# Kernel optimization log

Hardware: AMD Instinct MI355X
Metric: run time of the kernel (lower is better)

Reference implementation:

```python
import jax, jax.numpy as jnp
import numpy as np

N_NODES = 50000
N_EDGES = 600000
D_IN = 128
D_HID = 128


def _sage_conv(x, src, dst, n_nodes, W_l, b_l, W_r):
    """PyG SAGEConv: out = lin_l(mean_j x_j) + lin_r(x_i); lin_r has no bias."""
    msg = x[src]  # [E, D] gather from source nodes
    agg = jax.ops.segment_sum(msg, dst, num_segments=n_nodes)
    cnt = jax.ops.segment_sum(jnp.ones((msg.shape[0],), x.dtype), dst,
                              num_segments=n_nodes)
    mean = agg / jnp.maximum(cnt, 1.0)[:, None]
    return mean @ W_l + b_l + x @ W_r


def setup_inputs() -> dict:
    key = jax.random.key(0)
    ks = jax.random.split(key, 8)
    x = jax.random.normal(ks[0], (N_NODES, D_IN), dtype=jnp.float32)
    edge_index = jax.random.randint(ks[1], (2, N_EDGES), 0, N_NODES, dtype=jnp.int64)
    s1 = 1.0 / np.sqrt(D_IN)
    s2 = 1.0 / np.sqrt(D_HID)
    W1_l = jax.random.uniform(ks[2], (D_IN, D_HID), jnp.float32, -s1, s1)
    W1_r = jax.random.uniform(ks[3], (D_IN, D_HID), jnp.float32, -s1, s1)
    b1_l = jnp.zeros((D_HID,), jnp.float32)
    W2_l = jax.random.uniform(ks[4], (D_HID, D_HID), jnp.float32, -s2, s2)
    W2_r = jax.random.uniform(ks[5], (D_HID, D_HID), jnp.float32, -s2, s2)
    b2_l = jnp.zeros((D_HID,), jnp.float32)
    return {"x": x, "edge_index": edge_index,
            "W1_l": W1_l, "b1_l": b1_l, "W1_r": W1_r,
            "W2_l": W2_l, "b2_l": b2_l, "W2_r": W2_r}


def reference(x, edge_index, W1_l, b1_l, W1_r, W2_l, b2_l, W2_r):
    # forward (eval mode: dropout is identity)
    src, dst = edge_index[0], edge_index[1]
    n = x.shape[0]
    z = jax.nn.relu(_sage_conv(x, src, dst, n, W1_l, b1_l, W1_r))
    z = _sage_conv(z, src, dst, n, W2_l, b2_l, W2_r)
    return z
```

## Files before the change

### kernel.cpp

```cpp
#include <hip/hip_runtime.h>

typedef unsigned short ushort_t;
typedef __attribute__((ext_vector_type(8))) unsigned short ushort8;
typedef __attribute__((ext_vector_type(8))) __bf16 bf16x8;
typedef __attribute__((ext_vector_type(4))) float f32x4;

#define CAP 128

__device__ __forceinline__ ushort_t f2bf(float f) {
    union { float f; unsigned u; } v; v.f = f;
    unsigned r = v.u + 0x7FFFu + ((v.u >> 16) & 1u);
    return (ushort_t)(r >> 16);
}
__device__ __forceinline__ float bf2f(ushort_t b) {
    union { unsigned u; float f; } v; v.u = ((unsigned)b) << 16;
    return v.f;
}

__global__ __launch_bounds__(256) void prep_kernel(
    const float* __restrict__ x, ushort_t* __restrict__ xb,
    const float* __restrict__ W1l, const float* __restrict__ W1r,
    const float* __restrict__ W2l, const float* __restrict__ W2r,
    ushort_t* __restrict__ WT1, ushort_t* __restrict__ WT2,
    int* __restrict__ cnt, int n8, int n)
{
    int gid = blockIdx.x * 256 + threadIdx.x;
    if (gid < n) cnt[gid] = 0;
    if (gid < 65536) {
        int layer = gid >> 15;
        int id = gid & 32767;
        int k = id >> 7;
        int c = id & 127;
        const float* Wl = layer ? W2l : W1l;
        const float* Wr = layer ? W2r : W1r;
        ushort_t* WT = layer ? WT2 : WT1;
        float v = (k < 128) ? Wl[(size_t)k * 128 + c] : Wr[(size_t)(k - 128) * 128 + c];
        WT[(size_t)c * 256 + k] = f2bf(v);
    }
    if (gid >= n8) return;
    const float4 v0 = *(const float4*)&x[(size_t)gid * 8];
    const float4 v1 = *(const float4*)&x[(size_t)gid * 8 + 4];
    ushort8 r;
    r[0] = f2bf(v0.x); r[1] = f2bf(v0.y); r[2] = f2bf(v0.z); r[3] = f2bf(v0.w);
    r[4] = f2bf(v1.x); r[5] = f2bf(v1.y); r[6] = f2bf(v1.z); r[7] = f2bf(v1.w);
    *(ushort8*)&xb[(size_t)gid * 8] = r;
}

__global__ __launch_bounds__(256) void fill_bucket(
    const int* __restrict__ src, const int* __restrict__ dst,
    int* __restrict__ cnt, int* __restrict__ esrc, int E)
{
    int e = blockIdx.x * 256 + threadIdx.x;
    if (e < E) {
        int d = dst[e];
        int pos = atomicAdd(&cnt[d], 1);
        if (pos < CAP) esrc[(size_t)d * CAP + pos] = src[e];
    }
}

__global__ __launch_bounds__(256) void sage_layer(
    const ushort_t* __restrict__ feat,
    const int* __restrict__ esrc,
    const int* __restrict__ cnt,
    const ushort_t* __restrict__ WT,
    const float* __restrict__ bias,
    ushort_t* __restrict__ out_b,
    float* __restrict__ out_f,
    int n, int do_relu)
{
    __shared__ __align__(16) ushort_t a_lds[64 * 256];

    const int t = threadIdx.x;
    const int tile = blockIdx.x * 64;
    const int w = t >> 6;
    const int l = t & 63;
    const int l15 = l & 15;
    const int lg = l >> 4;

#pragma unroll
    for (int j = 0; j < 4; ++j) {
        int idx = t + j * 256;
        int r = idx >> 4;
        int g = 16 + (idx & 15);
        int gr = tile + r;
        ushort8 v = (ushort8)0;
        if (gr < n) v = *(const ushort8*)&feat[(size_t)gr * 128 + (idx & 15) * 8];
        int dstb = r * 512 + ((g * 16) ^ ((r & 7) << 4));
        *(ushort8*)((char*)a_lds + dstb) = v;
    }

    const int slot = lg;
    const int c = l15 << 3;
    for (int i = 0; i < 16; ++i) {
        int r = w * 16 + i;
        int node = tile + r;
        float a[8];
#pragma unroll
        for (int j = 0; j < 8; ++j) a[j] = 0.f;
        int d = 0;
        if (node < n) d = min(cnt[node], CAP);
        const size_t o = (size_t)node * CAP;

        for (int base = 0; base < d; base += 64) {
            const int m = min(d - base, 64);
            int idxv = (l < m) ? esrc[o + base + l] : 0;
            const int nit = (m + 3) >> 2;
            for (int ii = 0; ii < nit; ii += 4) {
                int e0 = (ii + 0) * 4 + slot;
                int e1 = (ii + 1) * 4 + slot;
                int e2 = (ii + 2) * 4 + slot;
                int e3 = (ii + 3) * 4 + slot;
                int s0 = __shfl(idxv, e0 & 63, 64);
                int s1 = __shfl(idxv, e1 & 63, 64);
                int s2 = __shfl(idxv, e2 & 63, 64);
                int s3 = __shfl(idxv, e3 & 63, 64);
                ushort8 r0 = *(const ushort8*)&feat[(size_t)s0 * 128 + c];
                ushort8 r1 = *(const ushort8*)&feat[(size_t)s1 * 128 + c];
                ushort8 r2 = *(const ushort8*)&feat[(size_t)s2 * 128 + c];
                ushort8 r3 = *(const ushort8*)&feat[(size_t)s3 * 128 + c];
                if (e0 < m) {
#pragma unroll
                    for (int j = 0; j < 8; ++j) a[j] += bf2f(r0[j]);
                }
                if (e1 < m) {
#pragma unroll
                    for (int j = 0; j < 8; ++j) a[j] += bf2f(r1[j]);
                }
                if (e2 < m) {
#pragma unroll
                    for (int j = 0; j < 8; ++j) a[j] += bf2f(r2[j]);
                }
                if (e3 < m) {
#pragma unroll
                    for (int j = 0; j < 8; ++j) a[j] += bf2f(r3[j]);
                }
            }
        }

#pragma unroll
        for (int j = 0; j < 8; ++j) {
            a[j] += __shfl_xor(a[j], 16, 64);
            a[j] += __shfl_xor(a[j], 32, 64);
        }

        if (slot == 0) {
            float sc = 1.0f / fmaxf((float)d, 1.0f);
            ushort8 rv;
#pragma unroll
            for (int j = 0; j < 8; ++j) rv[j] = f2bf(a[j] * sc);
            int dstb = r * 512 + ((l15 * 16) ^ ((r & 7) << 4));
            *(ushort8*)((char*)a_lds + dstb) = rv;
        }
    }
    __syncthreads();

    bf16x8 bfrag[2][8];
    {
        const ushort_t* p0 = &WT[(size_t)(w * 32 + l15) * 256 + lg * 8];
        const ushort_t* p1 = p0 + 16 * 256;
#pragma unroll
        for (int ks = 0; ks < 8; ++ks) {
            bfrag[0][ks] = *(const bf16x8*)(p0 + ks * 32);
            bfrag[1][ks] = *(const bf16x8*)(p1 + ks * 32);
        }
    }

    f32x4 acc[4][2];
#pragma unroll
    for (int rt = 0; rt < 4; ++rt)
#pragma unroll
        for (int ct = 0; ct < 2; ++ct)
#pragma unroll
            for (int i = 0; i < 4; ++i) acc[rt][ct][i] = 0.f;

#pragma unroll
    for (int ks = 0; ks < 8; ++ks) {
        bf16x8 af[4];
#pragma unroll
        for (int rt = 0; rt < 4; ++rt) {
            int r = rt * 16 + l15;
            int byteoff = r * 512 + (((ks * 64) + lg * 16) ^ ((r & 7) << 4));
            af[rt] = *(const bf16x8*)((const char*)a_lds + byteoff);
        }
#pragma unroll
        for (int rt = 0; rt < 4; ++rt)
#pragma unroll
            for (int ct = 0; ct < 2; ++ct)
                acc[rt][ct] = __builtin_amdgcn_mfma_f32_16x16x32_bf16(
                    af[rt], bfrag[ct][ks], acc[rt][ct], 0, 0, 0);
    }

#pragma unroll
    for (int ct = 0; ct < 2; ++ct) {
        int col = w * 32 + ct * 16 + l15;
        float bv = bias[col];
#pragma unroll
        for (int rt = 0; rt < 4; ++rt) {
#pragma unroll
            for (int i = 0; i < 4; ++i) {
                int row = tile + rt * 16 + lg * 4 + i;
                if (row < n) {
                    float v = acc[rt][ct][i] + bv;
                    if (do_relu) v = fmaxf(v, 0.f);
                    if (out_b) out_b[(size_t)row * 128 + col] = f2bf(v);
                    else       out_f[(size_t)row * 128 + col] = v;
                }
            }
        }
    }
}

extern "C" void kernel_launch(void* const* d_in, const int* in_sizes, int n_in,
                              void* d_out, int out_size, void* d_ws, size_t ws_size,
                              hipStream_t stream) {
    const float* x   = (const float*)d_in[0];
    const int*   ei  = (const int*)d_in[1];
    const float* W1l = (const float*)d_in[2];
    const float* b1l = (const float*)d_in[3];
    const float* W1r = (const float*)d_in[4];
    const float* W2l = (const float*)d_in[5];
    const float* b2l = (const float*)d_in[6];
    const float* W2r = (const float*)d_in[7];
    float* out = (float*)d_out;

    const int N = in_sizes[0] / 128;
    const int E = in_sizes[1] / 2;
    const int* src = ei;
    const int* dst = ei + E;

    char* ws = (char*)d_ws;
    ushort_t* xb  = (ushort_t*)ws;  ws += (size_t)N * 128 * sizeof(ushort_t);
    ushort_t* h1b = (ushort_t*)ws;  ws += (size_t)N * 128 * sizeof(ushort_t);
    ushort_t* WT1 = (ushort_t*)ws;  ws += 32768 * sizeof(ushort_t);
    ushort_t* WT2 = (ushort_t*)ws;  ws += 32768 * sizeof(ushort_t);
    int* cnt  = (int*)ws;  ws += (size_t)N * sizeof(int);
    int* esrc = (int*)ws;  ws += (size_t)N * CAP * sizeof(int);

    const int n8 = N * 128 / 8;
    prep_kernel<<<(n8 + 255) / 256, 256, 0, stream>>>(x, xb, W1l, W1r, W2l, W2r,
                                                      WT1, WT2, cnt, n8, N);

    fill_bucket<<<(E + 255) / 256, 256, 0, stream>>>(src, dst, cnt, esrc, E);

    const int nblk = (N + 63) / 64;

    sage_layer<<<nblk, 256, 0, stream>>>(xb, esrc, cnt, WT1, b1l, h1b, nullptr, N, 1);

    sage_layer<<<nblk, 256, 0, stream>>>(h1b, esrc, cnt, WT2, b2l, nullptr, out, N, 0);
}
```

Baseline: 216.1 us.

## Halve node tile to 32 and preload edge indices as int4 per slot

Shrinks each block's node tile from 64 to 32, which doubles the grid and halves LDS use and MFMA row tiles per block. Each wave now aggregates 8 nodes instead of 16. Every lane preloads its first four neighbor indices as int4 vectors, replacing the per-node shuffle-based index distribution. Neighbors beyond 16 are read directly with vector loads. This is meant to add occupancy and memory-level parallelism for the gather, at the cost of reloading the weight fragments in twice as many blocks.

New measurement: 218.5 us. About the same (+1.1%).

```diff
diff --git a/kernel.cpp b/kernel.cpp
--- a/kernel.cpp
+++ b/kernel.cpp
@@ -6,6 +6,7 @@
 typedef __attribute__((ext_vector_type(4))) float f32x4;
 
 #define CAP 128
+#define BN 32
 
 __device__ __forceinline__ ushort_t f2bf(float f) {
     union { float f; unsigned u; } v; v.f = f;
@@ -68,69 +69,99 @@
     float* __restrict__ out_f,
     int n, int do_relu)
 {
-    __shared__ __align__(16) ushort_t a_lds[64 * 256];
+    __shared__ __align__(16) ushort_t a_lds[BN * 256];
 
     const int t = threadIdx.x;
-    const int tile = blockIdx.x * 64;
+    const int tile = blockIdx.x * BN;
     const int w = t >> 6;
     const int l = t & 63;
     const int l15 = l & 15;
     const int lg = l >> 4;
-
-#pragma unroll
-    for (int j = 0; j < 4; ++j) {
+    const int slot = lg;
+    const int c = l15 << 3;
+
+#pragma unroll
+    for (int j = 0; j < 2; ++j) {
         int idx = t + j * 256;
         int r = idx >> 4;
-        int g = 16 + (idx & 15);
+        int g16 = idx & 15;
         int gr = tile + r;
         ushort8 v = (ushort8)0;
-        if (gr < n) v = *(const ushort8*)&feat[(size_t)gr * 128 + (idx & 15) * 8];
-        int dstb = r * 512 + ((g * 16) ^ ((r & 7) << 4));
+        if (gr < n) v = *(const ushort8*)&feat[(size_t)gr * 128 + g16 * 8];
+        int dstb = r * 512 + (((16 + g16) * 16) ^ ((r & 7) << 4));
         *(ushort8*)((char*)a_lds + dstb) = v;
     }
 
-    const int slot = lg;
-    const int c = l15 << 3;
-    for (int i = 0; i < 16; ++i) {
-        int r = w * 16 + i;
-        int node = tile + r;
+    const int nbase = tile + w * 8;
+    int dv = 0;
+    if (l < 8 && nbase + l < n) dv = cnt[nbase + l];
+
+    int4 iv[8];
+#pragma unroll
+    for (int i = 0; i < 8; ++i) {
+        if (nbase + i < n)
+            iv[i] = *(const int4*)(esrc + (size_t)(nbase + i) * CAP + slot * 4);
+    }
+
+#pragma unroll
+    for (int i = 0; i < 8; ++i) {
+        int node = nbase + i;
+        if (node >= n) break;
+        int d = min(__shfl(dv, i, 64), CAP);
+        const int* bp = esrc + (size_t)node * CAP;
+
         float a[8];
 #pragma unroll
         for (int j = 0; j < 8; ++j) a[j] = 0.f;
-        int d = 0;
-        if (node < n) d = min(cnt[node], CAP);
-        const size_t o = (size_t)node * CAP;
-
-        for (int base = 0; base < d; base += 64) {
-            const int m = min(d - base, 64);
-            int idxv = (l < m) ? esrc[o + base + l] : 0;
-            const int nit = (m + 3) >> 2;
-            for (int ii = 0; ii < nit; ii += 4) {
-                int e0 = (ii + 0) * 4 + slot;
-                int e1 = (ii + 1) * 4 + slot;
-                int e2 = (ii + 2) * 4 + slot;
-                int e3 = (ii + 3) * 4 + slot;
-                int s0 = __shfl(idxv, e0 & 63, 64);
-                int s1 = __shfl(idxv, e1 & 63, 64);
-                int s2 = __shfl(idxv, e2 & 63, 64);
-                int s3 = __shfl(idxv, e3 & 63, 64);
+
+        if (slot * 4 < d) {
+            int e0 = slot * 4;
+            int s0 = iv[i].x;
+            int s1 = (e0 + 1 < d) ? iv[i].y : s0;
+            int s2 = (e0 + 2 < d) ? iv[i].z : s0;
+            int s3 = (e0 + 3 < d) ? iv[i].w : s0;
+            ushort8 r0 = *(const ushort8*)&feat[(size_t)s0 * 128 + c];
+            ushort8 r1 = *(const ushort8*)&feat[(size_t)s1 * 128 + c];
+            ushort8 r2 = *(const ushort8*)&feat[(size_t)s2 * 128 + c];
+            ushort8 r3 = *(const ushort8*)&feat[(size_t)s3 * 128 + c];
+#pragma unroll
+            for (int j = 0; j < 8; ++j) a[j] += bf2f(r0[j]);
+            if (e0 + 1 < d) {
+#pragma unroll
+                for (int j = 0; j < 8; ++j) a[j] += bf2f(r1[j]);
+            }
+            if (e0 + 2 < d) {
+#pragma unroll
+                for (int j = 0; j < 8; ++j) a[j] += bf2f(r2[j]);
+            }
+            if (e0 + 3 < d) {
+#pragma unroll
+                for (int j = 0; j < 8; ++j) a[j] += bf2f(r3[j]);
+            }
+        }
+        for (int cb = 16; cb < d; cb += 16) {
+            int e0 = cb + slot * 4;
+            if (e0 < d) {
+                int4 v2 = *(const int4*)(bp + e0);
+                int s0 = v2.x;
+                int s1 = (e0 + 1 < d) ? v2.y : s0;
+                int s2 = (e0 + 2 < d) ? v2.z : s0;
+                int s3 = (e0 + 3 < d) ? v2.w : s0;
                 ushort8 r0 = *(const ushort8*)&feat[(size_t)s0 * 128 + c];
                 ushort8 r1 = *(const ushort8*)&feat[(size_t)s1 * 128 + c];
                 ushort8 r2 = *(const ushort8*)&feat[(size_t)s2 * 128 + c];
                 ushort8 r3 = *(const ushort8*)&feat[(size_t)s3 * 128 + c];
-                if (e0 < m) {
-#pragma unroll
-                    for (int j = 0; j < 8; ++j) a[j] += bf2f(r0[j]);
-                }
-                if (e1 < m) {
+#pragma unroll
+                for (int j = 0; j < 8; ++j) a[j] += bf2f(r0[j]);
+                if (e0 + 1 < d) {
 #pragma unroll
                     for (int j = 0; j < 8; ++j) a[j] += bf2f(r1[j]);
                 }
-                if (e2 < m) {
+                if (e0 + 2 < d) {
 #pragma unroll
                     for (int j = 0; j < 8; ++j) a[j] += bf2f(r2[j]);
                 }
-                if (e3 < m) {
+                if (e0 + 3 < d) {
 #pragma unroll
                     for (int j = 0; j < 8; ++j) a[j] += bf2f(r3[j]);
                 }
@@ -148,6 +179,7 @@
             ushort8 rv;
 #pragma unroll
             for (int j = 0; j < 8; ++j) rv[j] = f2bf(a[j] * sc);
+            int r = w * 8 + i;
             int dstb = r * 512 + ((l15 * 16) ^ ((r & 7) << 4));
             *(ushort8*)((char*)a_lds + dstb) = rv;
         }
@@ -165,9 +197,9 @@
         }
     }
 
-    f32x4 acc[4][2];
-#pragma unroll
-    for (int rt = 0; rt < 4; ++rt)
+    f32x4 acc[2][2];
+#pragma unroll
+    for (int rt = 0; rt < 2; ++rt)
 #pragma unroll
         for (int ct = 0; ct < 2; ++ct)
 #pragma unroll
@@ -175,15 +207,15 @@
 
 #pragma unroll
     for (int ks = 0; ks < 8; ++ks) {
-        bf16x8 af[4];
-#pragma unroll
-        for (int rt = 0; rt < 4; ++rt) {
+        bf16x8 af[2];
+#pragma unroll
+        for (int rt = 0; rt < 2; ++rt) {
             int r = rt * 16 + l15;
             int byteoff = r * 512 + (((ks * 64) + lg * 16) ^ ((r & 7) << 4));
             af[rt] = *(const bf16x8*)((const char*)a_lds + byteoff);
         }
 #pragma unroll
-        for (int rt = 0; rt < 4; ++rt)
+        for (int rt = 0; rt < 2; ++rt)
 #pragma unroll
             for (int ct = 0; ct < 2; ++ct)
                 acc[rt][ct] = __builtin_amdgcn_mfma_f32_16x16x32_bf16(
@@ -195,7 +227,7 @@
         int col = w * 32 + ct * 16 + l15;
         float bv = bias[col];
 #pragma unroll
-        for (int rt = 0; rt < 4; ++rt) {
+        for (int rt = 0; rt < 2; ++rt) {
 #pragma unroll
             for (int i = 0; i < 4; ++i) {
                 int row = tile + rt * 16 + lg * 4 + i;
@@ -242,7 +274,7 @@
 
     fill_bucket<<<(E + 255) / 256, 256, 0, stream>>>(src, dst, cnt, esrc, E);
 
-    const int nblk = (N + 63) / 64;
+    const int nblk = (N + BN - 1) / BN;
 
     sage_layer<<<nblk, 256, 0, stream>>>(xb, esrc, cnt, WT1, b1l, h1b, nullptr, N, 1);
 
```

## Gather one node per 16-lane group with prefetched neighbor indices, 32-row tiles

Applied to the files above, without the earlier changes.

Changes the neighbor-aggregation mapping so each 16-lane group owns a whole node and walks its edge list with int4 index loads, prefetching the next batch of four. This replaces the wave-wide shuffle scheme and removes the cross-slot reductions. The tile shrinks to 32 rows per block, which doubles the block count and halves the LDS use, so occupancy and load balance should improve. In exchange the weight fragments are reloaded for twice as many blocks, and lanes within a wave diverge when the four nodes have different degrees.

After: 198.6 us. 1.09x faster.

```diff
diff --git a/kernel.cpp b/kernel.cpp
--- a/kernel.cpp
+++ b/kernel.cpp
@@ -6,6 +6,7 @@
 typedef __attribute__((ext_vector_type(4))) float f32x4;
 
 #define CAP 128
+#define BN 32
 
 __device__ __forceinline__ ushort_t f2bf(float f) {
     union { float f; unsigned u; } v; v.f = f;
@@ -68,90 +69,87 @@
     float* __restrict__ out_f,
     int n, int do_relu)
 {
-    __shared__ __align__(16) ushort_t a_lds[64 * 256];
+    __shared__ __align__(16) ushort_t a_lds[BN * 256];
 
     const int t = threadIdx.x;
-    const int tile = blockIdx.x * 64;
+    const int tile = blockIdx.x * BN;
     const int w = t >> 6;
     const int l = t & 63;
     const int l15 = l & 15;
     const int lg = l >> 4;
-
-#pragma unroll
-    for (int j = 0; j < 4; ++j) {
+    const int c = l15 << 3;
+
+#pragma unroll
+    for (int j = 0; j < 2; ++j) {
         int idx = t + j * 256;
         int r = idx >> 4;
-        int g = 16 + (idx & 15);
+        int g16 = idx & 15;
         int gr = tile + r;
         ushort8 v = (ushort8)0;
-        if (gr < n) v = *(const ushort8*)&feat[(size_t)gr * 128 + (idx & 15) * 8];
-        int dstb = r * 512 + ((g * 16) ^ ((r & 7) << 4));
+        if (gr < n) v = *(const ushort8*)&feat[(size_t)gr * 128 + g16 * 8];
+        int dstb = r * 512 + (((16 + g16) * 16) ^ ((r & 7) << 4));
         *(ushort8*)((char*)a_lds + dstb) = v;
     }
 
-    const int slot = lg;
-    const int c = l15 << 3;
-    for (int i = 0; i < 16; ++i) {
-        int r = w * 16 + i;
-        int node = tile + r;
-        float a[8];
-#pragma unroll
-        for (int j = 0; j < 8; ++j) a[j] = 0.f;
-        int d = 0;
-        if (node < n) d = min(cnt[node], CAP);
-        const size_t o = (size_t)node * CAP;
-
-        for (int base = 0; base < d; base += 64) {
-            const int m = min(d - base, 64);
-            int idxv = (l < m) ? esrc[o + base + l] : 0;
-            const int nit = (m + 3) >> 2;
-            for (int ii = 0; ii < nit; ii += 4) {
-                int e0 = (ii + 0) * 4 + slot;
-                int e1 = (ii + 1) * 4 + slot;
-                int e2 = (ii + 2) * 4 + slot;
-                int e3 = (ii + 3) * 4 + slot;
-                int s0 = __shfl(idxv, e0 & 63, 64);
-                int s1 = __shfl(idxv, e1 & 63, 64);
-                int s2 = __shfl(idxv, e2 & 63, 64);
-                int s3 = __shfl(idxv, e3 & 63, 64);
-                ushort8 r0 = *(const ushort8*)&feat[(size_t)s0 * 128 + c];
-                ushort8 r1 = *(const ushort8*)&feat[(size_t)s1 * 128 + c];
-                ushort8 r2 = *(const ushort8*)&feat[(size_t)s2 * 128 + c];
-                ushort8 r3 = *(const ushort8*)&feat[(size_t)s3 * 128 + c];
-                if (e0 < m) {
-#pragma unroll
-                    for (int j = 0; j < 8; ++j) a[j] += bf2f(r0[j]);
-                }
-                if (e1 < m) {
-#pragma unroll
-                    for (int j = 0; j < 8; ++j) a[j] += bf2f(r1[j]);
-                }
-                if (e2 < m) {
-#pragma unroll
-                    for (int j = 0; j < 8; ++j) a[j] += bf2f(r2[j]);
-                }
-                if (e3 < m) {
-#pragma unroll
-                    for (int j = 0; j < 8; ++j) a[j] += bf2f(r3[j]);
-                }
-            }
-        }
-
-#pragma unroll
-        for (int j = 0; j < 8; ++j) {
-            a[j] += __shfl_xor(a[j], 16, 64);
-            a[j] += __shfl_xor(a[j], 32, 64);
-        }
-
-        if (slot == 0) {
-            float sc = 1.0f / fmaxf((float)d, 1.0f);
-            ushort8 rv;
-#pragma unroll
-            for (int j = 0; j < 8; ++j) rv[j] = f2bf(a[j] * sc);
-            int dstb = r * 512 + ((l15 * 16) ^ ((r & 7) << 4));
-            *(ushort8*)((char*)a_lds + dstb) = rv;
-        }
-    }
+    const int r0_ = w * 8 + lg;
+    const int r1_ = r0_ + 4;
+    const int node0 = tile + r0_;
+    const int node1 = tile + r1_;
+    const int* bp0 = esrc + (size_t)node0 * CAP;
+    const int* bp1 = esrc + (size_t)node1 * CAP;
+    int d0 = (node0 < n) ? min(cnt[node0], CAP) : 0;
+    int d1 = (node1 < n) ? min(cnt[node1], CAP) : 0;
+    int4 q0, q1;
+    if (d0 > 0) q0 = *(const int4*)bp0;
+    if (d1 > 0) q1 = *(const int4*)bp1;
+
+#define GATHER_NODE(rloc, dd, bp, qfirst)                                       \
+    {                                                                           \
+        float a[8];                                                             \
+        _Pragma("unroll")                                                       \
+        for (int j = 0; j < 8; ++j) a[j] = 0.f;                                 \
+        int4 q = qfirst;                                                        \
+        for (int cb = 0; cb < dd; cb += 4) {                                    \
+            int4 qn;                                                            \
+            if (cb + 4 < dd) qn = *(const int4*)((bp) + cb + 4);                \
+            int s0 = q.x;                                                       \
+            int s1 = (cb + 1 < dd) ? q.y : s0;                                  \
+            int s2 = (cb + 2 < dd) ? q.z : s0;                                  \
+            int s3 = (cb + 3 < dd) ? q.w : s0;                                  \
+            ushort8 v0 = *(const ushort8*)&feat[(size_t)s0 * 128 + c];          \
+            ushort8 v1 = *(const ushort8*)&feat[(size_t)s1 * 128 + c];          \
+            ushort8 v2 = *(const ushort8*)&feat[(size_t)s2 * 128 + c];          \
+            ushort8 v3 = *(const ushort8*)&feat[(size_t)s3 * 128 + c];          \
+            _Pragma("unroll")                                                   \
+            for (int j = 0; j < 8; ++j) a[j] += bf2f(v0[j]);                    \
+            if (cb + 1 < dd) {                                                  \
+                _Pragma("unroll")                                               \
+                for (int j = 0; j < 8; ++j) a[j] += bf2f(v1[j]);                \
+            }                                                                   \
+            if (cb + 2 < dd) {                                                  \
+                _Pragma("unroll")                                               \
+                for (int j = 0; j < 8; ++j) a[j] += bf2f(v2[j]);                \
+            }                                                                   \
+            if (cb + 3 < dd) {                                                  \
+                _Pragma("unroll")                                               \
+                for (int j = 0; j < 8; ++j) a[j] += bf2f(v3[j]);                \
+            }                                                                   \
+            q = qn;                                                             \
+        }                                                                       \
+        if (tile + (rloc) < n) {                                                \
+            float sc = 1.0f / fmaxf((float)(dd), 1.0f);                         \
+            ushort8 rv;                                                         \
+            _Pragma("unroll")                                                   \
+            for (int j = 0; j < 8; ++j) rv[j] = f2bf(a[j] * sc);                \
+            int dstb = (rloc) * 512 + ((l15 * 16) ^ (((rloc) & 7) << 4));       \
+            *(ushort8*)((char*)a_lds + dstb) = rv;                              \
+        }                                                                       \
+    }
+
+    GATHER_NODE(r0_, d0, bp0, q0)
+    GATHER_NODE(r1_, d1, bp1, q1)
+#undef GATHER_NODE
+
     __syncthreads();
 
     bf16x8 bfrag[2][8];
@@ -165,9 +163,9 @@
         }
     }
 
-    f32x4 acc[4][2];
-#pragma unroll
-    for (int rt = 0; rt < 4; ++rt)
+    f32x4 acc[2][2];
+#pragma unroll
+    for (int rt = 0; rt < 2; ++rt)
 #pragma unroll
         for (int ct = 0; ct < 2; ++ct)
 #pragma unroll
@@ -175,15 +173,15 @@
 
 #pragma unroll
     for (int ks = 0; ks < 8; ++ks) {
-        bf16x8 af[4];
-#pragma unroll
-        for (int rt = 0; rt < 4; ++rt) {
+        bf16x8 af[2];
+#pragma unroll
+        for (int rt = 0; rt < 2; ++rt) {
             int r = rt * 16 + l15;
             int byteoff = r * 512 + (((ks * 64) + lg * 16) ^ ((r & 7) << 4));
             af[rt] = *(const bf16x8*)((const char*)a_lds + byteoff);
         }
 #pragma unroll
-        for (int rt = 0; rt < 4; ++rt)
+        for (int rt = 0; rt < 2; ++rt)
 #pragma unroll
             for (int ct = 0; ct < 2; ++ct)
                 acc[rt][ct] = __builtin_amdgcn_mfma_f32_16x16x32_bf16(
@@ -195,7 +193,7 @@
         int col = w * 32 + ct * 16 + l15;
         float bv = bias[col];
 #pragma unroll
-        for (int rt = 0; rt < 4; ++rt) {
+        for (int rt = 0; rt < 2; ++rt) {
 #pragma unroll
             for (int i = 0; i < 4; ++i) {
                 int row = tile + rt * 16 + lg * 4 + i;
@@ -242,7 +240,7 @@
 
     fill_bucket<<<(E + 255) / 256, 256, 0, stream>>>(src, dst, cnt, esrc, E);
 
-    const int nblk = (N + 63) / 64;
+    const int nblk = (N + BN - 1) / BN;
 
     sage_layer<<<nblk, 256, 0, stream>>>(xb, esrc, cnt, WT1, b1l, h1b, nullptr, N, 1);
 
```
